# Optimization experiments

Measured on AMD Instinct MI355X. Metric: run time of the kernel, lower is better.

The kernel has to match this reference:

```python
import jax, jax.numpy as jnp
import numpy as np

OUT_FEATURES = 11008
IN_FEATURES = 4096
GROUP_SIZE = 32
NUM_GROUPS = OUT_FEATURES * IN_FEATURES // GROUP_SIZE        # 1,409,024
NUM_PACKED = NUM_GROUPS * (GROUP_SIZE // 8 * 3)              # 16,908,288 bytes


def block_dequantize_3bit(weight_q3, weight_norm):
    """Unpack 3-bit codes (8 values per 3 bytes) and dequantize to fp32."""
    p = weight_q3.reshape(-1, 3).astype(jnp.int32)  # [N/8, 3] bytes
    b0, b1, b2 = p[:, 0], p[:, 1], p[:, 2]
    q = jnp.stack([
        b0 & 7,
        (b0 >> 3) & 7,
        ((b0 >> 6) & 3) | ((b1 & 1) << 2),
        (b1 >> 1) & 7,
        (b1 >> 4) & 7,
        ((b1 >> 7) & 1) | ((b2 & 3) << 1),
        (b2 >> 2) & 7,
        (b2 >> 5) & 7,
    ], axis=-1)                                     # [N/8, 8] codes in 0..7
    q = q.reshape(NUM_GROUPS, GROUP_SIZE).astype(jnp.float32)
    norm = weight_norm.astype(jnp.float32)[:, None]  # [num_groups, 1]
    w = (q / 7.0) * 2.0 * norm - norm                # map [0,7] -> [-norm, norm]
    return w.reshape(OUT_FEATURES, IN_FEATURES)


def setup_inputs() -> dict:
    key = jax.random.key(0)
    k1, k2, k3, k4 = jax.random.split(key, 4)
    x = jax.random.normal(k1, (4, 128, IN_FEATURES), dtype=jnp.float32)
    weight_q3 = jax.random.randint(k2, (NUM_PACKED,), 0, 256, dtype=jnp.int32)
    weight_norm = (jax.random.uniform(k3, (NUM_GROUPS,), dtype=jnp.float32) * 0.1 + 0.01).astype(jnp.float16)
    bias = jax.random.normal(k4, (OUT_FEATURES,), dtype=jnp.float32) * 0.02
    return {"x": x, "weight_q3": weight_q3, "weight_norm": weight_norm, "bias": bias}


def reference(x, weight_q3, weight_norm, bias):
    w = block_dequantize_3bit(weight_q3, weight_norm)  # [out, in] fp32
    return jnp.einsum('bsd,od->bso', x, w) + bias
```

## Files before the change

### kernel.cpp

```cpp
#include <hip/hip_runtime.h>
#include <hip/hip_fp16.h>

#define M_TOTAL 512
#define N_TOTAL 11008
#define K_TOTAL 4096
#define BM 128
#define BN 64
#define BK 64
#define NT (K_TOTAL / BK)
#define NUM_GROUPS (N_TOTAL * K_TOTAL / 32)
#define LDK 72

typedef short bf16x8 __attribute__((ext_vector_type(8)));
typedef _Float16 f16x8 __attribute__((ext_vector_type(8)));
typedef float f32x4 __attribute__((ext_vector_type(4)));

__device__ __forceinline__ unsigned int pack2_bf16(float f0, float f1) {
    unsigned int u0 = __builtin_bit_cast(unsigned int, f0) + 0x8000u;
    unsigned int u1 = __builtin_bit_cast(unsigned int, f1) + 0x8000u;
    return (u0 >> 16) | (u1 & 0xFFFF0000u);
}

__device__ __forceinline__ void async_ld16(void* lds, const void* g) {
    __builtin_amdgcn_global_load_lds(
        (const __attribute__((address_space(1))) unsigned int*)g,
        (__attribute__((address_space(3))) unsigned int*)lds, 16, 0, 0);
}

__device__ __forceinline__ int detect_mode_wave(const void* __restrict__ wn) {
    const int lane = threadIdx.x & 63;
    const unsigned short* u16 = (const unsigned short*)wn;
    const float* f32p = (const float*)wn;
    const float vb = __builtin_bit_cast(float, (unsigned int)u16[lane] << 16);
    const float vh = __half2float(__builtin_bit_cast(__half, u16[lane]));
    const float vf = f32p[lane];
    const unsigned long long mb = __ballot(vb > 0.005f && vb < 0.12f);
    const unsigned long long mh = __ballot(vh > 0.005f && vh < 0.12f);
    (void)vf;
    return (mb == ~0ull) ? 2 : ((mh == ~0ull) ? 1 : 0);
}

__global__ void __launch_bounds__(256)
convert_x_kernel(const float* __restrict__ x, unsigned short* __restrict__ xh) {
    const int i = (blockIdx.x * 256 + threadIdx.x) * 4;
    const float4 v = *(const float4*)&x[i];
    const unsigned int p0 = __builtin_bit_cast(unsigned int, __builtin_amdgcn_cvt_pkrtz(v.x, v.y));
    const unsigned int p1 = __builtin_bit_cast(unsigned int, __builtin_amdgcn_cvt_pkrtz(v.z, v.w));
    *(uint2*)&xh[i] = make_uint2(p0, p1);
}

__global__ void __launch_bounds__(512)
norm_pack_kernel(const void* __restrict__ wn, unsigned int* __restrict__ np) {
    const int mode = detect_mode_wave(wn);
    const int g = blockIdx.x * 512 + threadIdx.x;
    if (g >= NUM_GROUPS) return;
    float n;
    if (mode == 0)      n = ((const float*)wn)[g];
    else if (mode == 1) n = __half2float(((const __half*)wn)[g]);
    else                n = __builtin_bit_cast(float,
                            (unsigned int)((const unsigned short*)wn)[g] << 16);
    np[g] = __builtin_bit_cast(unsigned int,
                __builtin_amdgcn_cvt_pkrtz(n * (2.0f / 7.0f), -n));
}

__global__ void __launch_bounds__(512, 6)
l3b_gemm_pipe(const _Float16* __restrict__ xh, const int* __restrict__ wq,
              const unsigned int* __restrict__ np, const float* __restrict__ bias,
              float* __restrict__ out)
{
    __shared__ _Float16 As[2][BM * 64];
    __shared__ _Float16 Bs[2][BN * 64];

    const int tid  = threadIdx.x;

    const int bid = blockIdx.x;
    const int w   = (bid & 7) * 86 + (bid >> 3);
    const int m0  = (w & 3) * BM;
    const int n0  = (w >> 2) * BN;

    const int wid  = tid >> 6;
    const int lane = tid & 63;
    const int quad = lane >> 4;
    const int lm   = lane & 15;
    const int wm   = (wid >> 1) * 32;
    const int wn_  = (wid & 1) * 32;

    const int arow0 = wid * 8 + (lane >> 3);
    const int acol  = ((lane & 7) ^ ((lane >> 3) & 7)) * 8;
    const int aphys = (lane & 7) * 8;

    const int gl   = tid >> 2;
    const int sub  = tid & 3;
    const int bn_l = gl >> 1;
    const int kg   = gl & 1;
    const int ldsB = (bn_l << 6) + (((kg * 4 + sub) ^ (bn_l & 7)) << 3);

    auto stageA = [&](int it, int buf) {
#pragma unroll
        for (int j = 0; j < 2; ++j) {
            const int row = arow0 + j * 64;
            async_ld16((void*)&As[buf][(row << 6) + aphys],
                       &xh[(size_t)(m0 + row) * K_TOTAL + it * 64 + acol]);
        }
    };

    auto loadB = [&](int it, int& b0, int& b1, int& b2, unsigned int& npk) {
        const int g    = (n0 + bn_l) * (K_TOTAL / 32) + it * 2 + kg;
        const int base = g * 12 + sub * 3;
        b0 = wq[base]; b1 = wq[base + 1]; b2 = wq[base + 2];
        npk = np[g];
    };

    const __half2 h1024 = __builtin_bit_cast(__half2, 0x64006400u);
    auto decodeB = [&](int b0, int b1, int b2, unsigned int npk, int buf) {
        const __half2 ss = __builtin_bit_cast(__half2,
            __builtin_amdgcn_perm(npk, npk, 0x01000100u));
        const __half2 cc = __builtin_bit_cast(__half2,
            __builtin_amdgcn_perm(npk, npk, 0x03020302u));
        const unsigned int bits =
            (unsigned)b0 | ((unsigned)b1 << 8) | ((unsigned)b2 << 16);
        unsigned int packs[4];
#pragma unroll
        for (int j = 0; j < 4; ++j) {
            const unsigned int q0 = (bits >> (6 * j)) & 7;
            const unsigned int q1 = (bits >> (6 * j + 3)) & 7;
            const __half2 h = __builtin_bit_cast(__half2,
                (q0 | (q1 << 16)) | 0x64006400u);
            const __half2 q = __hsub2(h, h1024);
            packs[j] = __builtin_bit_cast(unsigned int, __hfma2(q, ss, cc));
        }
        *(uint4*)&Bs[buf][ldsB] = make_uint4(packs[0], packs[1], packs[2], packs[3]);
    };

    f32x4 acc[2][2];
#pragma unroll
    for (int i = 0; i < 2; ++i)
#pragma unroll
        for (int j = 0; j < 2; ++j) acc[i][j] = (f32x4){0.f, 0.f, 0.f, 0.f};

    auto mfmaTile = [&](const _Float16* Asb, const _Float16* Bsb) {
#pragma unroll
        for (int ks = 0; ks < 2; ++ks) {
            const int cswz = (((ks * 4 + quad) ^ (lm & 7)) << 3);
            f16x8 aF[2], bF[2];
#pragma unroll
            for (int mi = 0; mi < 2; ++mi)
                aF[mi] = *(const f16x8*)&Asb[((wm + mi * 16 + lm) << 6) + cswz];
#pragma unroll
            for (int ni = 0; ni < 2; ++ni)
                bF[ni] = *(const f16x8*)&Bsb[((wn_ + ni * 16 + lm) << 6) + cswz];
#pragma unroll
            for (int mi = 0; mi < 2; ++mi)
#pragma unroll
                for (int ni = 0; ni < 2; ++ni)
                    acc[mi][ni] = __builtin_amdgcn_mfma_f32_16x16x32_f16(
                        aF[mi], bF[ni], acc[mi][ni], 0, 0, 0);
        }
    };

    int a0, a1, a2; unsigned int an;
    int b0, b1, b2; unsigned int bn;
    int c0, c1, c2; unsigned int cn;
    int d0, d1, d2; unsigned int dn;

    loadB(0, a0, a1, a2, an);
    loadB(1, b0, b1, b2, bn);
    loadB(2, c0, c1, c2, cn);
    stageA(0, 0);
    decodeB(a0, a1, a2, an, 0);
    __syncthreads();

    for (int it = 0; it < NT; it += 4) {
        {
            const int t = it;
            if (t + 1 < NT) stageA(t + 1, 1);
            if (t + 3 < NT) loadB(t + 3, d0, d1, d2, dn);
            if (t + 1 < NT) decodeB(b0, b1, b2, bn, 1);
            mfmaTile(As[0], Bs[0]);
            __syncthreads();
        }
        {
            const int t = it + 1;
            if (t + 1 < NT) stageA(t + 1, 0);
            if (t + 3 < NT) loadB(t + 3, a0, a1, a2, an);
            if (t + 1 < NT) decodeB(c0, c1, c2, cn, 0);
            mfmaTile(As[1], Bs[1]);
            __syncthreads();
        }
        {
            const int t = it + 2;
            if (t + 1 < NT) stageA(t + 1, 1);
            if (t + 3 < NT) loadB(t + 3, b0, b1, b2, bn);
            if (t + 1 < NT) decodeB(d0, d1, d2, dn, 1);
            mfmaTile(As[0], Bs[0]);
            __syncthreads();
        }
        {
            const int t = it + 3;
            if (t + 1 < NT) stageA(t + 1, 0);
            if (t + 3 < NT) loadB(t + 3, c0, c1, c2, cn);
            if (t + 1 < NT) decodeB(a0, a1, a2, an, 0);
            mfmaTile(As[1], Bs[1]);
            __syncthreads();
        }
    }

#pragma unroll
    for (int ni = 0; ni < 2; ++ni) {
        const int o  = n0 + wn_ + ni * 16 + lm;
        const float bv = bias[o];
#pragma unroll
        for (int mi = 0; mi < 2; ++mi) {
#pragma unroll
            for (int r = 0; r < 4; ++r) {
                const int m = m0 + wm + mi * 16 + quad * 4 + r;
                out[m * N_TOTAL + o] = acc[mi][ni][r] + bv;
            }
        }
    }
}

__global__ void __launch_bounds__(256)
l3b_gemm_kernel(const float* __restrict__ x, const int* __restrict__ wq,
                const void* __restrict__ wnorm, const float* __restrict__ bias,
                float* __restrict__ out)
{
    __shared__ unsigned short As[128 * LDK];
    __shared__ unsigned short Bs[64 * LDK];

    const int mode = detect_mode_wave(wnorm);
    const int tid  = threadIdx.x;
    const int m0   = blockIdx.y * 128;
    const int n0   = blockIdx.x * 64;
    const int wid  = tid >> 6;
    const int lane = tid & 63;
    const int quad = lane >> 4;
    const int lm   = lane & 15;
    const int wm   = (wid >> 1) * 64;
    const int wn   = (wid & 1) * 32;

    f32x4 acc[4][2];
#pragma unroll
    for (int i = 0; i < 4; ++i)
#pragma unroll
        for (int j = 0; j < 2; ++j) acc[i][j] = (f32x4){0.f, 0.f, 0.f, 0.f};

    const int ar = tid >> 4;
    const int ac = (tid & 15) * 4;
    const int gin      = tid >> 1;
    const int half     = tid & 1;
    const int bn_local = gin >> 1;
    const int bkg      = gin & 1;

    for (int it = 0; it < NT; ++it) {
        const int k0 = it * BK;
        __syncthreads();
#pragma unroll
        for (int p = 0; p < 8; ++p) {
            const int row = p * 16 + ar;
            const float4 v = *(const float4*)&x[(m0 + row) * K_TOTAL + k0 + ac];
            *(uint2*)&As[row * LDK + ac] =
                make_uint2(pack2_bf16(v.x, v.y), pack2_bf16(v.z, v.w));
        }
        {
            const int g    = (n0 + bn_local) * (K_TOTAL / 32) + it * 2 + bkg;
            const int base = g * 12 + half * 6;
            const int2 w0 = *(const int2*)&wq[base];
            const int2 w1 = *(const int2*)&wq[base + 2];
            const int2 w2 = *(const int2*)&wq[base + 4];
            float nrm;
            if (mode == 0)      nrm = ((const float*)wnorm)[g];
            else if (mode == 1) nrm = __half2float(((const __half*)wnorm)[g]);
            else                nrm = __builtin_bit_cast(float,
                                    (unsigned int)((const unsigned short*)wnorm)[g] << 16);
            const float a = nrm * (2.0f / 7.0f);
            const float b = -nrm;
            const unsigned int bits0 =
                (unsigned)w0.x | ((unsigned)w0.y << 8) | ((unsigned)w1.x << 16);
            const unsigned int bits1 =
                (unsigned)w1.y | ((unsigned)w2.x << 8) | ((unsigned)w2.y << 16);
            unsigned int packs[8];
#pragma unroll
            for (int t3 = 0; t3 < 2; ++t3) {
                const unsigned int bits = t3 ? bits1 : bits0;
#pragma unroll
                for (int j = 0; j < 4; ++j) {
                    const float f0 = fmaf((float)((bits >> (6 * j)) & 7), a, b);
                    const float f1 = fmaf((float)((bits >> (6 * j + 3)) & 7), a, b);
                    packs[t3 * 4 + j] = pack2_bf16(f0, f1);
                }
            }
            unsigned int* dst = (unsigned int*)&Bs[bn_local * LDK + bkg * 32 + half * 16];
            *(uint4*)dst       = make_uint4(packs[0], packs[1], packs[2], packs[3]);
            *(uint4*)(dst + 4) = make_uint4(packs[4], packs[5], packs[6], packs[7]);
        }
        __syncthreads();
#pragma unroll
        for (int ks = 0; ks < 2; ++ks) {
            const int kb = ks * 32 + quad * 8;
            bf16x8 aF[4], bF[2];
#pragma unroll
            for (int mi = 0; mi < 4; ++mi)
                aF[mi] = *(const bf16x8*)&As[(wm + mi * 16 + lm) * LDK + kb];
#pragma unroll
            for (int ni = 0; ni < 2; ++ni)
                bF[ni] = *(const bf16x8*)&Bs[(wn + ni * 16 + lm) * LDK + kb];
#pragma unroll
            for (int mi = 0; mi < 4; ++mi)
#pragma unroll
                for (int ni = 0; ni < 2; ++ni)
                    acc[mi][ni] = __builtin_amdgcn_mfma_f32_16x16x32_bf16(
                        aF[mi], bF[ni], acc[mi][ni], 0, 0, 0);
        }
    }
#pragma unroll
    for (int ni = 0; ni < 2; ++ni) {
        const int o  = n0 + wn + ni * 16 + lm;
        const float bv = bias[o];
#pragma unroll
        for (int mi = 0; mi < 4; ++mi)
#pragma unroll
            for (int r = 0; r < 4; ++r) {
                const int m = m0 + wm + mi * 16 + quad * 4 + r;
                out[m * N_TOTAL + o] = acc[mi][ni][r] + bv;
            }
    }
}

extern "C" void kernel_launch(void* const* d_in, const int* in_sizes, int n_in,
                              void* d_out, int out_size, void* d_ws, size_t ws_size,
                              hipStream_t stream) {
    const float* x    = (const float*)d_in[0];
    const int*   wq   = (const int*)d_in[1];
    const void*  wn   = d_in[2];
    const float* bias = (const float*)d_in[3];
    float* out = (float*)d_out;

    const size_t xh_off = 256;
    const size_t xh_sz  = (size_t)M_TOTAL * K_TOTAL * 2;
    const size_t np_off = xh_off + xh_sz;
    const size_t np_sz  = (size_t)NUM_GROUPS * 4;
    const size_t need   = np_off + np_sz;

    if (ws_size >= need) {
        unsigned short* xh = (unsigned short*)((char*)d_ws + xh_off);
        unsigned int*   np = (unsigned int*)((char*)d_ws + np_off);
        convert_x_kernel<<<(M_TOTAL * K_TOTAL / 4) / 256, 256, 0, stream>>>(x, xh);
        norm_pack_kernel<<<(NUM_GROUPS + 511) / 512, 512, 0, stream>>>(wn, np);
        l3b_gemm_pipe<<<(M_TOTAL / BM) * (N_TOTAL / BN), 512, 0, stream>>>(
            (const _Float16*)xh, wq, np, bias, out);
    } else {
        dim3 grid(N_TOTAL / 64, M_TOTAL / 128);
        l3b_gemm_kernel<<<grid, 256, 0, stream>>>(x, wq, wn, bias, out);
    }
}
```

Baseline: 202.2 us.

## Pre-transpose activations for direct register loads and use 32x32 MFMA

The fp16 conversion kernel now also rearranges x into a k-chunk-major layout, so each wave can read its A fragments straight from global memory into registers. This removes the A tile from shared memory and its async LDS staging. The GEMM switches from four 16x16x32 MFMAs per k-step to 32x32x16 MFMAs with one 16-element accumulator, and the occupancy hint drops from 6 to 5. Without A in LDS, the kernel relies on L2 and register prefetch to reuse A across blocks, which raises global load traffic and register pressure.

```diff
diff --git a/kernel.cpp b/kernel.cpp
--- a/kernel.cpp
+++ b/kernel.cpp
@@ -14,17 +14,12 @@
 typedef short bf16x8 __attribute__((ext_vector_type(8)));
 typedef _Float16 f16x8 __attribute__((ext_vector_type(8)));
 typedef float f32x4 __attribute__((ext_vector_type(4)));
+typedef float f32x16 __attribute__((ext_vector_type(16)));
 
 __device__ __forceinline__ unsigned int pack2_bf16(float f0, float f1) {
     unsigned int u0 = __builtin_bit_cast(unsigned int, f0) + 0x8000u;
     unsigned int u1 = __builtin_bit_cast(unsigned int, f1) + 0x8000u;
     return (u0 >> 16) | (u1 & 0xFFFF0000u);
-}
-
-__device__ __forceinline__ void async_ld16(void* lds, const void* g) {
-    __builtin_amdgcn_global_load_lds(
-        (const __attribute__((address_space(1))) unsigned int*)g,
-        (__attribute__((address_space(3))) unsigned int*)lds, 16, 0, 0);
 }
 
 __device__ __forceinline__ int detect_mode_wave(const void* __restrict__ wn) {
@@ -41,12 +36,30 @@
 }
 
 __global__ void __launch_bounds__(256)
-convert_x_kernel(const float* __restrict__ x, unsigned short* __restrict__ xh) {
-    const int i = (blockIdx.x * 256 + threadIdx.x) * 4;
-    const float4 v = *(const float4*)&x[i];
-    const unsigned int p0 = __builtin_bit_cast(unsigned int, __builtin_amdgcn_cvt_pkrtz(v.x, v.y));
-    const unsigned int p1 = __builtin_bit_cast(unsigned int, __builtin_amdgcn_cvt_pkrtz(v.z, v.w));
-    *(uint2*)&xh[i] = make_uint2(p0, p1);
+convert_x_t_kernel(const float* __restrict__ x, unsigned short* __restrict__ xt) {
+    __shared__ unsigned short tile[32][72];
+    const int t  = threadIdx.x;
+    const int mb = (blockIdx.x & 15) * 32;
+    const int kb = (blockIdx.x >> 4) * 64;
+    {
+        const int m  = t >> 3;
+        const int kq = t & 7;
+        const float* src = &x[(size_t)(mb + m) * K_TOTAL + kb + kq * 8];
+        const float4 v0 = *(const float4*)src;
+        const float4 v1 = *(const float4*)(src + 4);
+        unsigned int p0 = __builtin_bit_cast(unsigned int, __builtin_amdgcn_cvt_pkrtz(v0.x, v0.y));
+        unsigned int p1 = __builtin_bit_cast(unsigned int, __builtin_amdgcn_cvt_pkrtz(v0.z, v0.w));
+        unsigned int p2 = __builtin_bit_cast(unsigned int, __builtin_amdgcn_cvt_pkrtz(v1.x, v1.y));
+        unsigned int p3 = __builtin_bit_cast(unsigned int, __builtin_amdgcn_cvt_pkrtz(v1.z, v1.w));
+        *(uint4*)&tile[m][kq * 8] = make_uint4(p0, p1, p2, p3);
+    }
+    __syncthreads();
+    {
+        const int kc = t >> 5;
+        const int mm = t & 31;
+        const uint4 v = *(const uint4*)&tile[mm][kc * 8];
+        *(uint4*)&xt[(size_t)((kb >> 3) + kc) * (M_TOTAL * 8) + (size_t)(mb + mm) * 8] = v;
+    }
 }
 
 __global__ void __launch_bounds__(512)
@@ -63,13 +76,13 @@
                 __builtin_amdgcn_cvt_pkrtz(n * (2.0f / 7.0f), -n));
 }
 
-__global__ void __launch_bounds__(512, 6)
+__global__ void __launch_bounds__(512, 5)
 l3b_gemm_pipe(const _Float16* __restrict__ xh, const int* __restrict__ wq,
               const unsigned int* __restrict__ np, const float* __restrict__ bias,
               float* __restrict__ out)
 {
-    __shared__ _Float16 As[2][BM * 64];
-    __shared__ _Float16 Bs[2][BN * 64];
+    __shared__ _Float16 Bs0[BN * 64];
+    __shared__ _Float16 Bs1[BN * 64];
 
     const int tid  = threadIdx.x;
 
@@ -80,14 +93,10 @@
 
     const int wid  = tid >> 6;
     const int lane = tid & 63;
-    const int quad = lane >> 4;
-    const int lm   = lane & 15;
+    const int lr   = lane & 31;
+    const int lh   = lane >> 5;
     const int wm   = (wid >> 1) * 32;
     const int wn_  = (wid & 1) * 32;
-
-    const int arow0 = wid * 8 + (lane >> 3);
-    const int acol  = ((lane & 7) ^ ((lane >> 3) & 7)) * 8;
-    const int aphys = (lane & 7) * 8;
 
     const int gl   = tid >> 2;
     const int sub  = tid & 3;
@@ -95,13 +104,14 @@
     const int kg   = gl & 1;
     const int ldsB = (bn_l << 6) + (((kg * 4 + sub) ^ (bn_l & 7)) << 3);
 
-    auto stageA = [&](int it, int buf) {
-#pragma unroll
-        for (int j = 0; j < 2; ++j) {
-            const int row = arow0 + j * 64;
-            async_ld16((void*)&As[buf][(row << 6) + aphys],
-                       &xh[(size_t)(m0 + row) * K_TOTAL + it * 64 + acol]);
-        }
+    const _Float16* aBase = xh + (size_t)(m0 + wm + lr) * 8;
+
+    auto loadA = [&](int it, f16x8& a0, f16x8& a1, f16x8& a2, f16x8& a3) {
+        const _Float16* p = aBase + (size_t)(it * 8 + lh) * (M_TOTAL * 8);
+        a0 = *(const f16x8*)(p);
+        a1 = *(const f16x8*)(p + 2 * (M_TOTAL * 8));
+        a2 = *(const f16x8*)(p + 4 * (M_TOTAL * 8));
+        a3 = *(const f16x8*)(p + 6 * (M_TOTAL * 8));
     };
 
     auto loadB = [&](int it, int& b0, int& b1, int& b2, unsigned int& npk) {
@@ -112,7 +122,7 @@
     };
 
     const __half2 h1024 = __builtin_bit_cast(__half2, 0x64006400u);
-    auto decodeB = [&](int b0, int b1, int b2, unsigned int npk, int buf) {
+    auto decodeB = [&](int b0, int b1, int b2, unsigned int npk, _Float16* Bb) {
         const __half2 ss = __builtin_bit_cast(__half2,
             __builtin_amdgcn_perm(npk, npk, 0x01000100u));
         const __half2 cc = __builtin_bit_cast(__half2,
@@ -129,94 +139,81 @@
             const __half2 q = __hsub2(h, h1024);
             packs[j] = __builtin_bit_cast(unsigned int, __hfma2(q, ss, cc));
         }
-        *(uint4*)&Bs[buf][ldsB] = make_uint4(packs[0], packs[1], packs[2], packs[3]);
+        *(uint4*)&Bb[ldsB] = make_uint4(packs[0], packs[1], packs[2], packs[3]);
     };
 
-    f32x4 acc[2][2];
-#pragma unroll
-    for (int i = 0; i < 2; ++i)
-#pragma unroll
-        for (int j = 0; j < 2; ++j) acc[i][j] = (f32x4){0.f, 0.f, 0.f, 0.f};
-
-    auto mfmaTile = [&](const _Float16* Asb, const _Float16* Bsb) {
-#pragma unroll
-        for (int ks = 0; ks < 2; ++ks) {
-            const int cswz = (((ks * 4 + quad) ^ (lm & 7)) << 3);
-            f16x8 aF[2], bF[2];
-#pragma unroll
-            for (int mi = 0; mi < 2; ++mi)
-                aF[mi] = *(const f16x8*)&Asb[((wm + mi * 16 + lm) << 6) + cswz];
-#pragma unroll
-            for (int ni = 0; ni < 2; ++ni)
-                bF[ni] = *(const f16x8*)&Bsb[((wn_ + ni * 16 + lm) << 6) + cswz];
-#pragma unroll
-            for (int mi = 0; mi < 2; ++mi)
-#pragma unroll
-                for (int ni = 0; ni < 2; ++ni)
-                    acc[mi][ni] = __builtin_amdgcn_mfma_f32_16x16x32_f16(
-                        aF[mi], bF[ni], acc[mi][ni], 0, 0, 0);
-        }
+    f32x16 acc = {};
+
+    const int bRow  = wn_ + lr;
+    const int bOff  = bRow << 6;
+    const int bSwz  = bRow & 7;
+
+    auto mfmaTile = [&](const _Float16* Bb, const f16x8& a0, const f16x8& a1,
+                        const f16x8& a2, const f16x8& a3) {
+        f16x8 bF0 = *(const f16x8*)&Bb[bOff + (((0 + lh) ^ bSwz) << 3)];
+        f16x8 bF1 = *(const f16x8*)&Bb[bOff + (((2 + lh) ^ bSwz) << 3)];
+        f16x8 bF2 = *(const f16x8*)&Bb[bOff + (((4 + lh) ^ bSwz) << 3)];
+        f16x8 bF3 = *(const f16x8*)&Bb[bOff + (((6 + lh) ^ bSwz) << 3)];
+        acc = __builtin_amdgcn_mfma_f32_32x32x16_f16(a0, bF0, acc, 0, 0, 0);
+        acc = __builtin_amdgcn_mfma_f32_32x32x16_f16(a1, bF1, acc, 0, 0, 0);
+        acc = __builtin_amdgcn_mfma_f32_32x32x16_f16(a2, bF2, acc, 0, 0, 0);
+        acc = __builtin_amdgcn_mfma_f32_32x32x16_f16(a3, bF3, acc, 0, 0, 0);
     };
 
-    int a0, a1, a2; unsigned int an;
-    int b0, b1, b2; unsigned int bn;
-    int c0, c1, c2; unsigned int cn;
-    int d0, d1, d2; unsigned int dn;
-
-    loadB(0, a0, a1, a2, an);
-    loadB(1, b0, b1, b2, bn);
-    loadB(2, c0, c1, c2, cn);
-    stageA(0, 0);
-    decodeB(a0, a1, a2, an, 0);
+    f16x8 aC0, aC1, aC2, aC3, aN0, aN1, aN2, aN3;
+    int w00, w01, w02; unsigned int n0p;
+    int w10, w11, w12; unsigned int n1p;
+    int w20, w21, w22; unsigned int n2p;
+    int w30, w31, w32; unsigned int n3p;
+
+    loadB(0, w00, w01, w02, n0p);
+    loadB(1, w10, w11, w12, n1p);
+    loadB(2, w20, w21, w22, n2p);
+    loadA(0, aC0, aC1, aC2, aC3);
+    decodeB(w00, w01, w02, n0p, Bs0);
     __syncthreads();
 
     for (int it = 0; it < NT; it += 4) {
         {
             const int t = it;
-            if (t + 1 < NT) stageA(t + 1, 1);
-            if (t + 3 < NT) loadB(t + 3, d0, d1, d2, dn);
-            if (t + 1 < NT) decodeB(b0, b1, b2, bn, 1);
-            mfmaTile(As[0], Bs[0]);
+            if (t + 1 < NT) loadA(t + 1, aN0, aN1, aN2, aN3);
+            if (t + 3 < NT) loadB(t + 3, w30, w31, w32, n3p);
+            if (t + 1 < NT) decodeB(w10, w11, w12, n1p, Bs1);
+            mfmaTile(Bs0, aC0, aC1, aC2, aC3);
             __syncthreads();
         }
         {
             const int t = it + 1;
-            if (t + 1 < NT) stageA(t + 1, 0);
-            if (t + 3 < NT) loadB(t + 3, a0, a1, a2, an);
-            if (t + 1 < NT) decodeB(c0, c1, c2, cn, 0);
-            mfmaTile(As[1], Bs[1]);
+            if (t + 1 < NT) loadA(t + 1, aC0, aC1, aC2, aC3);
+            if (t + 3 < NT) loadB(t + 3, w00, w01, w02, n0p);
+            if (t + 1 < NT) decodeB(w20, w21, w22, n2p, Bs0);
+            mfmaTile(Bs1, aN0, aN1, aN2, aN3);
             __syncthreads();
         }
         {
             const int t = it + 2;
-            if (t + 1 < NT) stageA(t + 1, 1);
-            if (t + 3 < NT) loadB(t + 3, b0, b1, b2, bn);
-            if (t + 1 < NT) decodeB(d0, d1, d2, dn, 1);
-            mfmaTile(As[0], Bs[0]);
+            if (t + 1 < NT) loadA(t + 1, aN0, aN1, aN2, aN3);
+            if (t + 3 < NT) loadB(t + 3, w10, w11, w12, n1p);
+            if (t + 1 < NT) decodeB(w30, w31, w32, n3p, Bs1);
+            mfmaTile(Bs0, aC0, aC1, aC2, aC3);
             __syncthreads();
         }
         {
             const int t = it + 3;
-            if (t + 1 < NT) stageA(t + 1, 0);
-            if (t + 3 < NT) loadB(t + 3, c0, c1, c2, cn);
-            if (t + 1 < NT) decodeB(a0, a1, a2, an, 0);
-            mfmaTile(As[1], Bs[1]);
+            if (t + 1 < NT) loadA(t + 1, aC0, aC1, aC2, aC3);
+            if (t + 3 < NT) loadB(t + 3, w20, w21, w22, n2p);
+            if (t + 1 < NT) decodeB(w00, w01, w02, n0p, Bs0);
+            mfmaTile(Bs1, aN0, aN1, aN2, aN3);
             __syncthreads();
         }
     }
 
-#pragma unroll
-    for (int ni = 0; ni < 2; ++ni) {
-        const int o  = n0 + wn_ + ni * 16 + lm;
-        const float bv = bias[o];
-#pragma unroll
-        for (int mi = 0; mi < 2; ++mi) {
-#pragma unroll
-            for (int r = 0; r < 4; ++r) {
-                const int m = m0 + wm + mi * 16 + quad * 4 + r;
-                out[m * N_TOTAL + o] = acc[mi][ni][r] + bv;
-            }
-        }
+    const int o  = n0 + wn_ + lr;
+    const float bv = bias[o];
+#pragma unroll
+    for (int r = 0; r < 16; ++r) {
+        const int m = m0 + wm + (r & 3) + ((r >> 2) << 3) + (lh << 2);
+        out[(size_t)m * N_TOTAL + o] = acc[r] + bv;
     }
 }
 
@@ -345,7 +342,7 @@
     if (ws_size >= need) {
         unsigned short* xh = (unsigned short*)((char*)d_ws + xh_off);
         unsigned int*   np = (unsigned int*)((char*)d_ws + np_off);
-        convert_x_kernel<<<(M_TOTAL * K_TOTAL / 4) / 256, 256, 0, stream>>>(x, xh);
+        convert_x_t_kernel<<<(M_TOTAL / 32) * (K_TOTAL / 64), 256, 0, stream>>>(x, xh);
         norm_pack_kernel<<<(NUM_GROUPS + 511) / 512, 512, 0, stream>>>(wn, np);
         l3b_gemm_pipe<<<(M_TOTAL / BM) * (N_TOTAL / BN), 512, 0, stream>>>(
             (const _Float16*)xh, wq, np, bias, out);
```

New measurement: 216.5 us. +7.1%, slower.

## Replace async global-to-LDS A loads with register-staged prefetch two tiles ahead

Applied to the files above, without the earlier changes.

A-tile staging no longer uses the direct global_load_lds path. It now loads the activation tile into registers two iterations ahead and writes it into LDS with a swizzled layout alongside the B decode. The aim is to hide global latency better and to swizzle on the LDS write side. In exchange, register pressure rises (four extra uint4 per thread) and the kernel issues extra LDS store instructions.

```diff
diff --git a/kernel.cpp b/kernel.cpp
--- a/kernel.cpp
+++ b/kernel.cpp
@@ -19,12 +19,6 @@
     unsigned int u0 = __builtin_bit_cast(unsigned int, f0) + 0x8000u;
     unsigned int u1 = __builtin_bit_cast(unsigned int, f1) + 0x8000u;
     return (u0 >> 16) | (u1 & 0xFFFF0000u);
-}
-
-__device__ __forceinline__ void async_ld16(void* lds, const void* g) {
-    __builtin_amdgcn_global_load_lds(
-        (const __attribute__((address_space(1))) unsigned int*)g,
-        (__attribute__((address_space(3))) unsigned int*)lds, 16, 0, 0);
 }
 
 __device__ __forceinline__ int detect_mode_wave(const void* __restrict__ wn) {
@@ -86,8 +80,9 @@
     const int wn_  = (wid & 1) * 32;
 
     const int arow0 = wid * 8 + (lane >> 3);
-    const int acol  = ((lane & 7) ^ ((lane >> 3) & 7)) * 8;
-    const int aphys = (lane & 7) * 8;
+    const int chunk = lane & 7;
+    const int aswz  = (chunk ^ (arow0 & 7)) * 8;
+    const _Float16* aPtr = xh + (size_t)(m0 + arow0) * K_TOTAL + chunk * 8;
 
     const int gl   = tid >> 2;
     const int sub  = tid & 3;
@@ -95,13 +90,14 @@
     const int kg   = gl & 1;
     const int ldsB = (bn_l << 6) + (((kg * 4 + sub) ^ (bn_l & 7)) << 3);
 
-    auto stageA = [&](int it, int buf) {
-#pragma unroll
-        for (int j = 0; j < 2; ++j) {
-            const int row = arow0 + j * 64;
-            async_ld16((void*)&As[buf][(row << 6) + aphys],
-                       &xh[(size_t)(m0 + row) * K_TOTAL + it * 64 + acol]);
-        }
+    auto loadA = [&](int it, uint4& u0, uint4& u1) {
+        const _Float16* p = aPtr + it * 64;
+        u0 = *(const uint4*)p;
+        u1 = *(const uint4*)(p + (size_t)64 * K_TOTAL);
+    };
+    auto writeA = [&](const uint4& u0, const uint4& u1, int buf) {
+        *(uint4*)&As[buf][(arow0 << 6) + aswz]        = u0;
+        *(uint4*)&As[buf][((arow0 + 64) << 6) + aswz] = u1;
     };
 
     auto loadB = [&](int it, int& b0, int& b1, int& b2, unsigned int& npk) {
@@ -158,48 +154,52 @@
         }
     };
 
-    int a0, a1, a2; unsigned int an;
-    int b0, b1, b2; unsigned int bn;
-    int c0, c1, c2; unsigned int cn;
-    int d0, d1, d2; unsigned int dn;
-
-    loadB(0, a0, a1, a2, an);
-    loadB(1, b0, b1, b2, bn);
-    loadB(2, c0, c1, c2, cn);
-    stageA(0, 0);
-    decodeB(a0, a1, a2, an, 0);
+    uint4 aP0, aP1;
+    uint4 aQ0, aQ1;
+    int w00, w01, w02; unsigned int n0p;
+    int w10, w11, w12; unsigned int n1p;
+    int w20, w21, w22; unsigned int n2p;
+    int w30, w31, w32; unsigned int n3p;
+
+    loadA(0, aP0, aP1);
+    loadB(0, w00, w01, w02, n0p);
+    loadB(1, w10, w11, w12, n1p);
+    loadB(2, w20, w21, w22, n2p);
+    writeA(aP0, aP1, 0);
+    decodeB(w00, w01, w02, n0p, 0);
+    loadA(1, aQ0, aQ1);
     __syncthreads();
 
     for (int it = 0; it < NT; it += 4) {
         {
             const int t = it;
-            if (t + 1 < NT) stageA(t + 1, 1);
-            if (t + 3 < NT) loadB(t + 3, d0, d1, d2, dn);
-            if (t + 1 < NT) decodeB(b0, b1, b2, bn, 1);
+            if (t + 2 < NT) loadA(t + 2, aP0, aP1);
+            if (t + 3 < NT) loadB(t + 3, w30, w31, w32, n3p);
+            if (t + 1 < NT) { writeA(aQ0, aQ1, 1); decodeB(w10, w11, w12, n1p, 1); }
             mfmaTile(As[0], Bs[0]);
             __syncthreads();
         }
         {
             const int t = it + 1;
-            if (t + 1 < NT) stageA(t + 1, 0);
-            if (t + 3 < NT) loadB(t + 3, a0, a1, a2, an);
-            if (t + 1 < NT) decodeB(c0, c1, c2, cn, 0);
+            if (t + 2 < NT) loadA(t + 2, aQ0, aQ1);
+            if (t + 3 < NT) loadB(t + 3, w00, w01, w02, n0p);
+            if (t + 1 < NT) { writeA(aP0, aP1, 0); decodeB(w20, w21, w22, n2p, 0); }
             mfmaTile(As[1], Bs[1]);
             __syncthreads();
         }
         {
             const int t = it + 2;
-            if (t + 1 < NT) stageA(t + 1, 1);
-            if (t + 3 < NT) loadB(t + 3, b0, b1, b2, bn);
-            if (t + 1 < NT) decodeB(d0, d1, d2, dn, 1);
+            if (t + 2 < NT) loadA(t + 2, aP0, aP1);
+            if (t + 3 < NT) loadB(t + 3, w10, w11, w12, n1p);
+            if (t + 1 < NT) { writeA(aQ0, aQ1, 1); decodeB(w30, w31, w32, n3p, 1); }
             mfmaTile(As[0], Bs[0]);
             __syncthreads();
         }
         {
             const int t = it + 3;
-            if (t + 1 < NT) stageA(t + 1, 0);
-            if (t + 3 < NT) loadB(t + 3, c0, c1, c2, cn);
-            if (t + 1 < NT) decodeB(a0, a1, a2, an, 0);
+            if (t + 2 < NT) loadA(t + 2, aQ0, aQ1);
+            if (t + 3 < NT) loadB(t + 3, w20, w21, w22, n2p);
+            if (t + 1 < NT) { writeA(aP0, aP1, 0); decodeB(w00, w01, w02, n0p, 0); }
             mfmaTile(As[1], Bs[1]);
             __syncthreads();
         }
```

New measurement: 222.4 us. +10.0%, slower.
